# Kernel optimization log

Hardware: AMD Instinct MI355X
Metric: run time of the kernel (lower is better)

## Reference

```python
import jax, jax.numpy as jnp
import numpy as np

B, L, D, S = 64, 1024, 1024, 32  # batch, tokens, feat dim, num attribute ids (labels 1..S; 0 = ignore)
EPS = 1e-8  # torch F.cosine_similarity eps


def setup_inputs() -> dict:
    key = jax.random.key(0)
    k1, k2, k3 = jax.random.split(key, 3)
    attributes = jax.random.randint(k1, (B, L), 0, S + 1, dtype=jnp.int32)
    # guarantee every label 1..S appears in each sample (so every segment mean is defined
    # and max(attribute) == S, matching the fixed-S vectorization of the original loop)
    attributes = attributes.at[:, :S].set(jnp.arange(1, S + 1, dtype=jnp.int32)[None, :])
    text_feats = jax.random.normal(k2, (B, L, D), dtype=jnp.float32)
    Vgs = jax.random.normal(k3, (B, S, D), dtype=jnp.float32)
    return {"attributes": attributes, "text_feats": text_feats, "Vgs": Vgs}


def reference(attributes, text_feats, Vgs):
    # one-hot over labels 1..S: [B, L, S]
    onehot = (attributes[..., None] == jnp.arange(1, S + 1, dtype=attributes.dtype)).astype(text_feats.dtype)
    # segment sums and counts -> per-attribute mean feature: [B, S, D]
    seg_sum = jnp.einsum('bls,bld->bsd', onehot, text_feats)
    seg_cnt = jnp.sum(onehot, axis=1)  # [B, S]
    seg_mean = seg_sum / seg_cnt[..., None]
    # cosine similarity per (sample, attribute), torch semantics with eps clamp
    num = jnp.sum(Vgs * seg_mean, axis=-1)  # [B, S]
    denom = jnp.maximum(jnp.linalg.norm(Vgs, axis=-1) * jnp.linalg.norm(seg_mean, axis=-1), EPS)
    cos = num / denom
    # per-sample: 1 - mean_over_attributes(cos); loss: mean over batch (count == B here)
    loss = jnp.mean(1.0 - jnp.mean(cos, axis=-1))
    return loss
```

## Files before the change

kernel.cpp:

```cpp
#include <hip/hip_runtime.h>

constexpr int Bx = 64;
constexpr int Lx = 1024;
constexpr int Dx = 1024;
constexpr int Sx = 32;

constexpr int DC   = 256;
constexpr int ROWS = Sx + 1;
constexpr int NBLK = Bx * (Dx / DC);
constexpr int PREF = 8;

__global__ __launch_bounds__(1024, 1) void seg_dot_kernel(
    const int*   __restrict__ attrs,
    const float* __restrict__ text,
    const float* __restrict__ vgs,
    float* __restrict__ pnum,
    float* __restrict__ pns2,
    float* __restrict__ pnv2,
    int*   __restrict__ wcnt)
{
    __shared__ float acc[ROWS * DC];
    __shared__ int   spack[Lx];
    __shared__ int   hist[ROWS];
    __shared__ int   cursor[ROWS];

    const int tid    = threadIdx.x;
    const int bid    = blockIdx.x;
    const int b      = bid >> 2;
    const int dchunk = bid & 3;
    const int d0     = dchunk * DC;

    for (int i = tid; i < ROWS * DC; i += 1024) acc[i] = 0.0f;
    if (tid < ROWS) hist[tid] = 0;
    __syncthreads();

    const int my_a = attrs[b * Lx + tid];
    atomicAdd(&hist[my_a], 1);
    __syncthreads();

    if (tid < 64) {
        const int h = (tid < ROWS) ? hist[tid] : 0;
        int v = h;
        #pragma unroll
        for (int off = 1; off < 64; off <<= 1) {
            const int u = __shfl_up(v, off, 64);
            if (tid >= off) v += u;
        }
        if (tid < ROWS) cursor[tid] = v - h;
    }
    __syncthreads();

    const int pos = atomicAdd(&cursor[my_a], 1);
    spack[pos] = (my_a << 16) | tid;
    if (dchunk == 0 && tid >= 1 && tid <= Sx) {
        wcnt[b * Sx + (tid - 1)] = hist[tid];
    }
    __syncthreads();

    const int w    = tid >> 6;
    const int lane = tid & 63;
    const float* __restrict__ tbase =
        text + (size_t)b * Lx * Dx + d0 + lane * 4;

    float4 a4  = make_float4(0.f, 0.f, 0.f, 0.f);
    int    cur = 0;

    for (int k0 = 0; k0 < 64; k0 += PREF) {
        int    pk[PREF];
        float4 v[PREF];
        #pragma unroll
        for (int j = 0; j < PREF; ++j)
            pk[j] = __builtin_amdgcn_readfirstlane(spack[w * 64 + k0 + j]);
        #pragma unroll
        for (int j = 0; j < PREF; ++j) {
            const int l = pk[j] & 0xffff;
            v[j] = *(const float4*)(tbase + (size_t)l * Dx);
        }
        #pragma unroll
        for (int j = 0; j < PREF; ++j) {
            const int s = pk[j] >> 16;
            if (s != cur) {
                atomicAdd(&acc[cur * DC + lane * 4 + 0], a4.x);
                atomicAdd(&acc[cur * DC + lane * 4 + 1], a4.y);
                atomicAdd(&acc[cur * DC + lane * 4 + 2], a4.z);
                atomicAdd(&acc[cur * DC + lane * 4 + 3], a4.w);
                a4  = make_float4(0.f, 0.f, 0.f, 0.f);
                cur = s;
            }
            if (s != 0) {
                a4.x += v[j].x; a4.y += v[j].y;
                a4.z += v[j].z; a4.w += v[j].w;
            }
        }
    }
    atomicAdd(&acc[cur * DC + lane * 4 + 0], a4.x);
    atomicAdd(&acc[cur * DC + lane * 4 + 1], a4.y);
    atomicAdd(&acc[cur * DC + lane * 4 + 2], a4.z);
    atomicAdd(&acc[cur * DC + lane * 4 + 3], a4.w);
    __syncthreads();

    #pragma unroll
    for (int si = 0; si < 2; ++si) {
        const int s = w + si * 16;
        const float4 vv =
            *(const float4*)(vgs + (size_t)(b * Sx + s) * Dx + d0 + lane * 4);
        const float4 m = *(const float4*)(&acc[(s + 1) * DC + lane * 4]);
        float num = m.x * vv.x + m.y * vv.y + m.z * vv.z + m.w * vv.w;
        float ns2 = m.x * m.x + m.y * m.y + m.z * m.z + m.w * m.w;
        float nv2 = vv.x * vv.x + vv.y * vv.y + vv.z * vv.z + vv.w * vv.w;
        #pragma unroll
        for (int off = 32; off > 0; off >>= 1) {
            num += __shfl_xor(num, off, 64);
            ns2 += __shfl_xor(ns2, off, 64);
            nv2 += __shfl_xor(nv2, off, 64);
        }
        if (lane == 0) {
            const int idx = bid * Sx + s;
            pnum[idx] = num;
            pns2[idx] = ns2;
            pnv2[idx] = nv2;
        }
    }
}

__global__ __launch_bounds__(256) void finalize_kernel(
    const float* __restrict__ pnum, const float* __restrict__ pns2,
    const float* __restrict__ pnv2, const int* __restrict__ wcnt,
    float* __restrict__ out)
{
    const int tid = threadIdx.x;
    float lsum = 0.0f;
    #pragma unroll
    for (int k = 0; k < (Bx * Sx) / 256; ++k) {
        const int p = k * 256 + tid;
        const int b = p >> 5;
        const int s = p & 31;
        float num = 0.f, ns2 = 0.f, nv2 = 0.f;
        #pragma unroll
        for (int dc = 0; dc < 4; ++dc) {
            const int idx = (b * 4 + dc) * Sx + s;
            num += pnum[idx];
            ns2 += pns2[idx];
            nv2 += pnv2[idx];
        }
        const float cnt   = (float)wcnt[p];
        const float denom = fmaxf(sqrtf(nv2) * sqrtf(ns2), 1e-8f * cnt);
        lsum += num / denom;
    }
    #pragma unroll
    for (int off = 32; off > 0; off >>= 1) lsum += __shfl_xor(lsum, off, 64);

    __shared__ float red[4];
    if ((tid & 63) == 0) red[tid >> 6] = lsum;
    __syncthreads();
    if (tid == 0) {
        const float total = red[0] + red[1] + red[2] + red[3];
        out[0] = 1.0f - total * (1.0f / (float)(Bx * Sx));
    }
}

extern "C" void kernel_launch(void* const* d_in, const int* in_sizes, int n_in,
                              void* d_out, int out_size, void* d_ws, size_t ws_size,
                              hipStream_t stream) {
    const int*   attrs = (const int*)d_in[0];
    const float* text  = (const float*)d_in[1];
    const float* vgs   = (const float*)d_in[2];
    float* out = (float*)d_out;

    float* pnum = (float*)d_ws;
    float* pns2 = pnum + NBLK * Sx;
    float* pnv2 = pns2 + NBLK * Sx;
    int*   wcnt = (int*)(pnv2 + NBLK * Sx);

    seg_dot_kernel<<<NBLK, 1024, 0, stream>>>(attrs, text, vgs,
                                              pnum, pns2, pnv2, wcnt);
    finalize_kernel<<<1, 256, 0, stream>>>(pnum, pns2, pnv2, wcnt, out);
}
```

Measured before the change: 371.1 us.

## Split label sort into separate kernel and pipeline narrower-chunk gather loads

Moves the per-sample counting sort of labels into its own kernel that writes packed indices to the workspace, so the main kernel no longer repeats the sort for every feature chunk. The main kernel uses 128-wide feature chunks (twice as many blocks, float2 loads) and a rolling software pipeline with a ring of prefetched rows, and it skips loads for ignored tokens. This costs one extra kernel launch and a global round-trip for the sorted indices. Narrower per-lane loads may reduce memory efficiency per request.

Result: no change. 370.6 us (-0.1%).

```diff
diff --git a/kernel.cpp b/kernel.cpp
--- a/kernel.cpp
+++ b/kernel.cpp
@@ -5,39 +5,27 @@
 constexpr int Dx = 1024;
 constexpr int Sx = 32;
 
-constexpr int DC   = 256;
+constexpr int DC   = 128;
+constexpr int NCH  = Dx / DC;
 constexpr int ROWS = Sx + 1;
-constexpr int NBLK = Bx * (Dx / DC);
+constexpr int NBLK = Bx * NCH;
 constexpr int PREF = 8;
 
-__global__ __launch_bounds__(1024, 1) void seg_dot_kernel(
-    const int*   __restrict__ attrs,
-    const float* __restrict__ text,
-    const float* __restrict__ vgs,
-    float* __restrict__ pnum,
-    float* __restrict__ pns2,
-    float* __restrict__ pnv2,
-    int*   __restrict__ wcnt)
+__global__ __launch_bounds__(1024) void sort_kernel(
+    const int* __restrict__ attrs,
+    int* __restrict__ spack_g,
+    int* __restrict__ wcnt)
 {
-    __shared__ float acc[ROWS * DC];
-    __shared__ int   spack[Lx];
-    __shared__ int   hist[ROWS];
-    __shared__ int   cursor[ROWS];
+    __shared__ int hist[ROWS];
+    __shared__ int cursor[ROWS];
+    const int b   = blockIdx.x;
+    const int tid = threadIdx.x;
 
-    const int tid    = threadIdx.x;
-    const int bid    = blockIdx.x;
-    const int b      = bid >> 2;
-    const int dchunk = bid & 3;
-    const int d0     = dchunk * DC;
-
-    for (int i = tid; i < ROWS * DC; i += 1024) acc[i] = 0.0f;
     if (tid < ROWS) hist[tid] = 0;
     __syncthreads();
-
-    const int my_a = attrs[b * Lx + tid];
-    atomicAdd(&hist[my_a], 1);
+    const int a = attrs[b * Lx + tid];
+    atomicAdd(&hist[a], 1);
     __syncthreads();
-
     if (tid < 64) {
         const int h = (tid < ROWS) ? hist[tid] : 0;
         int v = h;
@@ -49,65 +37,84 @@
         if (tid < ROWS) cursor[tid] = v - h;
     }
     __syncthreads();
+    const int pos = atomicAdd(&cursor[a], 1);
+    spack_g[b * Lx + pos] = (a << 16) | tid;
+    if (tid >= 1 && tid <= Sx) wcnt[b * Sx + (tid - 1)] = hist[tid];
+}
 
-    const int pos = atomicAdd(&cursor[my_a], 1);
-    spack[pos] = (my_a << 16) | tid;
-    if (dchunk == 0 && tid >= 1 && tid <= Sx) {
-        wcnt[b * Sx + (tid - 1)] = hist[tid];
-    }
+__global__ __launch_bounds__(1024, 8) void seg_dot_kernel(
+    const float* __restrict__ text,
+    const float* __restrict__ vgs,
+    const int*   __restrict__ spack_g,
+    float* __restrict__ pnum,
+    float* __restrict__ pns2,
+    float* __restrict__ pnv2)
+{
+    __shared__ float acc[ROWS * DC];
+
+    const int tid    = threadIdx.x;
+    const int bid    = blockIdx.x;
+    const int b      = bid >> 3;
+    const int dchunk = bid & 7;
+    const int d0     = dchunk * DC;
+    const int w      = tid >> 6;
+    const int lane   = tid & 63;
+
+    for (int i = tid; i < ROWS * DC; i += 1024) acc[i] = 0.0f;
+
+    const int pv = spack_g[b * Lx + w * 64 + lane];
+
+    const float* __restrict__ tbase =
+        text + (size_t)b * Lx * Dx + d0 + lane * 2;
+
     __syncthreads();
 
-    const int w    = tid >> 6;
-    const int lane = tid & 63;
-    const float* __restrict__ tbase =
-        text + (size_t)b * Lx * Dx + d0 + lane * 4;
+    float2 buf[PREF];
+    int    pk[PREF];
 
-    float4 a4  = make_float4(0.f, 0.f, 0.f, 0.f);
+    #pragma unroll
+    for (int j = 0; j < PREF; ++j) {
+        const int p = __builtin_amdgcn_readlane(pv, j);
+        pk[j] = p;
+        if (p >> 16) buf[j] = *(const float2*)(tbase + (size_t)(p & 0xffff) * Dx);
+    }
+
+    float2 a2  = make_float2(0.f, 0.f);
     int    cur = 0;
 
-    for (int k0 = 0; k0 < 64; k0 += PREF) {
-        int    pk[PREF];
-        float4 v[PREF];
-        #pragma unroll
-        for (int j = 0; j < PREF; ++j)
-            pk[j] = __builtin_amdgcn_readfirstlane(spack[w * 64 + k0 + j]);
-        #pragma unroll
-        for (int j = 0; j < PREF; ++j) {
-            const int l = pk[j] & 0xffff;
-            v[j] = *(const float4*)(tbase + (size_t)l * Dx);
+    #pragma unroll
+    for (int j = 0; j < 64; ++j) {
+        const int    slot = j & (PREF - 1);
+        const int    p    = pk[slot];
+        const int    s    = p >> 16;
+        const float2 vv   = buf[slot];
+        if (j + PREF < 64) {
+            const int pn = __builtin_amdgcn_readlane(pv, j + PREF);
+            pk[slot] = pn;
+            if (pn >> 16)
+                buf[slot] = *(const float2*)(tbase + (size_t)(pn & 0xffff) * Dx);
         }
-        #pragma unroll
-        for (int j = 0; j < PREF; ++j) {
-            const int s = pk[j] >> 16;
-            if (s != cur) {
-                atomicAdd(&acc[cur * DC + lane * 4 + 0], a4.x);
-                atomicAdd(&acc[cur * DC + lane * 4 + 1], a4.y);
-                atomicAdd(&acc[cur * DC + lane * 4 + 2], a4.z);
-                atomicAdd(&acc[cur * DC + lane * 4 + 3], a4.w);
-                a4  = make_float4(0.f, 0.f, 0.f, 0.f);
-                cur = s;
-            }
-            if (s != 0) {
-                a4.x += v[j].x; a4.y += v[j].y;
-                a4.z += v[j].z; a4.w += v[j].w;
-            }
+        if (s != cur) {
+            atomicAdd(&acc[cur * DC + lane * 2 + 0], a2.x);
+            atomicAdd(&acc[cur * DC + lane * 2 + 1], a2.y);
+            a2  = make_float2(0.f, 0.f);
+            cur = s;
         }
+        if (s != 0) { a2.x += vv.x; a2.y += vv.y; }
     }
-    atomicAdd(&acc[cur * DC + lane * 4 + 0], a4.x);
-    atomicAdd(&acc[cur * DC + lane * 4 + 1], a4.y);
-    atomicAdd(&acc[cur * DC + lane * 4 + 2], a4.z);
-    atomicAdd(&acc[cur * DC + lane * 4 + 3], a4.w);
+    atomicAdd(&acc[cur * DC + lane * 2 + 0], a2.x);
+    atomicAdd(&acc[cur * DC + lane * 2 + 1], a2.y);
     __syncthreads();
 
     #pragma unroll
     for (int si = 0; si < 2; ++si) {
         const int s = w + si * 16;
-        const float4 vv =
-            *(const float4*)(vgs + (size_t)(b * Sx + s) * Dx + d0 + lane * 4);
-        const float4 m = *(const float4*)(&acc[(s + 1) * DC + lane * 4]);
-        float num = m.x * vv.x + m.y * vv.y + m.z * vv.z + m.w * vv.w;
-        float ns2 = m.x * m.x + m.y * m.y + m.z * m.z + m.w * m.w;
-        float nv2 = vv.x * vv.x + vv.y * vv.y + vv.z * vv.z + vv.w * vv.w;
+        const float2 vv =
+            *(const float2*)(vgs + (size_t)(b * Sx + s) * Dx + d0 + lane * 2);
+        const float2 m = *(const float2*)(&acc[(s + 1) * DC + lane * 2]);
+        float num = m.x * vv.x + m.y * vv.y;
+        float ns2 = m.x * m.x + m.y * m.y;
+        float nv2 = vv.x * vv.x + vv.y * vv.y;
         #pragma unroll
         for (int off = 32; off > 0; off >>= 1) {
             num += __shfl_xor(num, off, 64);
@@ -137,8 +144,8 @@
         const int s = p & 31;
         float num = 0.f, ns2 = 0.f, nv2 = 0.f;
         #pragma unroll
-        for (int dc = 0; dc < 4; ++dc) {
-            const int idx = (b * 4 + dc) * Sx + s;
+        for (int dc = 0; dc < NCH; ++dc) {
+            const int idx = (b * NCH + dc) * Sx + s;
             num += pnum[idx];
             ns2 += pns2[idx];
             nv2 += pnv2[idx];
@@ -167,12 +174,14 @@
     const float* vgs   = (const float*)d_in[2];
     float* out = (float*)d_out;
 
-    float* pnum = (float*)d_ws;
-    float* pns2 = pnum + NBLK * Sx;
-    float* pnv2 = pns2 + NBLK * Sx;
-    int*   wcnt = (int*)(pnv2 + NBLK * Sx);
+    int*   spack = (int*)d_ws;
+    float* pnum  = (float*)(spack + Bx * Lx);
+    float* pns2  = pnum + NBLK * Sx;
+    float* pnv2  = pns2 + NBLK * Sx;
+    int*   wcnt  = (int*)(pnv2 + NBLK * Sx);
 
-    seg_dot_kernel<<<NBLK, 1024, 0, stream>>>(attrs, text, vgs,
-                                              pnum, pns2, pnv2, wcnt);
+    sort_kernel<<<Bx, 1024, 0, stream>>>(attrs, spack, wcnt);
+    seg_dot_kernel<<<NBLK, 1024, 0, stream>>>(text, vgs, spack,
+                                              pnum, pns2, pnv2);
     finalize_kernel<<<1, 256, 0, stream>>>(pnum, pns2, pnv2, wcnt, out);
 }
```
